# Performance work log

Hardware: AMD Instinct MI355X
Metric: run time of the kernel (lower is better)

The kernel has to match this reference:

```python
import jax, jax.numpy as jnp
import numpy as np

B, C, H, W, K = 4, 32, 192, 192, 3
BETA = 15.0   # soft-max temperature used by the repo's Morphology module
EPS = 1e-5    # BatchNorm eps
KK = K * K


def _window_taps(x, dil):
    """Zero-padded dilated KxK window taps, stacked on axis 0 -> (KK, B, C, H, W).
    Matches nn.Unfold(kernel_size=K, dilation=dil, padding=dil*(K//2))."""
    p = dil * (K // 2)
    xp = jnp.pad(x, ((0, 0), (0, 0), (p, p), (p, p)))
    return jnp.stack(
        [xp[:, :, i * dil:i * dil + H, j * dil:j * dil + W]
         for i in range(K) for j in range(K)], axis=0)


def _w_taps(w):
    # (C, K, K) -> (KK, 1, C, 1, 1) aligned with tap order i*K+j
    return w.reshape(C, KK).T[:, None, :, None, None]


def soft_dilate(x, w, dil):
    v = _window_taps(x, dil) + _w_taps(w)          # (KK,B,C,H,W)
    return jax.nn.logsumexp(BETA * v, axis=0) / BETA


def soft_erode(x, w, dil):
    v = _w_taps(w) - _window_taps(x, dil)
    return -(jax.nn.logsumexp(BETA * v, axis=0) / BETA)


def batchnorm(x, gamma, beta):
    mu = jnp.mean(x, axis=(0, 2, 3), keepdims=True)
    var = jnp.var(x, axis=(0, 2, 3), keepdims=True)
    xn = (x - mu) * jax.lax.rsqrt(var + EPS)
    return xn * gamma[None, :, None, None] + beta[None, :, None, None]


def setup_inputs() -> dict:
    key = jax.random.key(0)
    k1, k2, k3, k4 = jax.random.split(key, 4)
    return {
        "x": jax.random.normal(k1, (B, C, H, W), jnp.float32),
        "wd": jax.random.normal(k2, (4, C, K, K), jnp.float32) * 0.1,
        "we": jax.random.normal(k3, (4, C, K, K), jnp.float32) * 0.1,
        "gs": jnp.ones((4, C), jnp.float32),
        "bs": jnp.zeros((4, C), jnp.float32),
        "Wc": jax.random.normal(k4, (C, 4 * C), jnp.float32) * (1.0 / np.sqrt(4 * C)),
        "g": jnp.ones((C,), jnp.float32),
        "b": jnp.zeros((C,), jnp.float32),
    }


def reference(x, wd, we, gs, bs, Wc, g, b):
    branches = []
    for i in range(4):                      # fixed set of dilation factors 1..4
        d = i + 1
        y = soft_dilate(x, wd[i], d)        # soft morphological dilation
        y = soft_erode(y, we[i], d)         # then erosion => closing
        y = jax.nn.relu(batchnorm(y, gs[i], bs[i]))
        branches.append(y)
    xc = jnp.concatenate(branches, axis=1)  # (B, 4C, H, W)
    y = jnp.einsum('bihw,oi->bohw', xc, Wc) # 1x1 conv, no bias
    y = jax.nn.relu(batchnorm(y, g, b))
    return y                                 # Dropout2d is identity in eval
```

## Files before the change

kernel.cpp:

```cpp
#include <hip/hip_runtime.h>
#include <hip/hip_bf16.h>

#define B_   4
#define C_   32
#define H_   192
#define W_   192
#define HW_  (H_ * W_)
#define EPS_ 1e-5f

#define SCALE_IN  21.640425613334453f
#define SCALE_OUT 0.046209812037329687f

#define SPW 48
#define SQW 40

#define NP1 (128 * 576)
#define NP2 (32 * 288)

__device__ __forceinline__ float bf2f(unsigned short u) {
    return __uint_as_float((unsigned int)u << 16);
}
__device__ __forceinline__ unsigned short f2bf(float f) {
    const unsigned int u = __float_as_uint(f);
    return (unsigned short)((u + 0x7fffu + ((u >> 16) & 1u)) >> 16);
}

__device__ float          g_cw[2304];
__device__ float          g_Wt[4096];
__device__ float          g_stats[320];
__device__ float          g_p1[2 * NP1];
__device__ float          g_p2[2 * NP2];
__device__ __attribute__((aligned(16))) unsigned short g_E[(size_t)4 * B_ * C_ * HW_];
__device__ __attribute__((aligned(16))) unsigned short g_Yb[(size_t)B_ * C_ * HW_];

__global__ void prep_k(const float* __restrict__ wd, const float* __restrict__ we,
                       const float* __restrict__ Wc) {
    for (int i = threadIdx.x; i < 2304; i += 256) {
        const float v = (i < 1152) ? wd[i] : we[i - 1152];
        g_cw[i] = exp2f(SCALE_IN * v);
    }
    for (int i = threadIdx.x; i < 4096; i += 256) {
        const int ci = i >> 5;
        const int k  = i & 31;
        g_Wt[i] = Wc[(size_t)k * 128 + ci];
    }
}

template<int D>
__device__ __forceinline__ void morph_branch(int b, int c, int h0, int w0,
                                             int slotbase,
                                             const float* __restrict__ sP,
                                             float* __restrict__ sQ) {
    constexpr int QE   = 32 + 2 * D;
    constexpr int QEG  = (QE + 3) / 4;
    constexpr int UNITS = QE * QEG;
    constexpr int POFF = 8 - 2 * D;
    constexpr int AB   = POFF & ~3;
    constexpr int OFF  = POFF & 3;
    constexpr int NR   = (OFF + 2 * D + 4 + 3) / 4;
    constexpr int NR3  = (2 * D + 4 + 3) / 4;
    constexpr int br   = D - 1;

    const int tid = threadIdx.x;
    const int cb  = (br * C_ + c) * 9;

    {
        float cd[9];
#pragma unroll
        for (int k = 0; k < 9; k++) cd[k] = g_cw[cb + k];

#pragma unroll
        for (int it = 0; it < 2; ++it) {
            const int unit = tid + it * 256;
            if (unit < UNITS) {
                const int qi = unit / QEG;
                const int qj = (unit - qi * QEG) * 4;
                float a0 = 0.f, a1 = 0.f, a2 = 0.f, a3 = 0.f;
#pragma unroll
                for (int i = 0; i < 3; i++) {
                    const float* rp = &sP[(qi + 8 + (i - 2) * D) * SPW + qj + AB];
                    float buf[NR * 4];
#pragma unroll
                    for (int r = 0; r < NR; r++)
                        *(float4*)&buf[r * 4] = *(const float4*)&rp[r * 4];
#pragma unroll
                    for (int j = 0; j < 3; j++) {
                        const float wgt = cd[i * 3 + j];
                        a0 = fmaf(wgt, buf[OFF + j * D + 0], a0);
                        a1 = fmaf(wgt, buf[OFF + j * D + 1], a1);
                        a2 = fmaf(wgt, buf[OFF + j * D + 2], a2);
                        a3 = fmaf(wgt, buf[OFF + j * D + 3], a3);
                    }
                }
                float q0 = __builtin_amdgcn_rcpf(a0);
                float q1 = __builtin_amdgcn_rcpf(a1);
                float q2 = __builtin_amdgcn_rcpf(a2);
                float q3 = __builtin_amdgcn_rcpf(a3);
                const int hq = h0 - D + qi;
                const int wq = w0 - D + qj;
                const bool rowo = (hq < 0) || (hq >= H_);
                q0 = (rowo || (wq + 0 < 0) || (wq + 0 >= W_)) ? 1.0f : q0;
                q1 = (rowo || (wq + 1 < 0) || (wq + 1 >= W_)) ? 1.0f : q1;
                q2 = (rowo || (wq + 2 < 0) || (wq + 2 >= W_)) ? 1.0f : q2;
                q3 = (rowo || (wq + 3 < 0) || (wq + 3 >= W_)) ? 1.0f : q3;
                *(float4*)&sQ[qi * SQW + qj] = make_float4(q0, q1, q2, q3);
            }
        }
    }
    __syncthreads();

    {
        float ce[9];
#pragma unroll
        for (int k = 0; k < 9; k++) ce[k] = g_cw[1152 + cb + k];

        const int oi = tid >> 3;
        const int oj = (tid & 7) * 4;
        float t0 = 0.f, t1 = 0.f, t2 = 0.f, t3 = 0.f;
#pragma unroll
        for (int i = 0; i < 3; i++) {
            const float* rq = &sQ[(oi + i * D) * SQW + oj];
            float buf[NR3 * 4];
#pragma unroll
            for (int r = 0; r < NR3; r++)
                *(float4*)&buf[r * 4] = *(const float4*)&rq[r * 4];
#pragma unroll
            for (int j = 0; j < 3; j++) {
                const float wgt = ce[i * 3 + j];
                t0 = fmaf(wgt, buf[j * D + 0], t0);
                t1 = fmaf(wgt, buf[j * D + 1], t1);
                t2 = fmaf(wgt, buf[j * D + 2], t2);
                t3 = fmaf(wgt, buf[j * D + 3], t3);
            }
        }
        const float e0 = -SCALE_OUT * log2f(t0);
        const float e1 = -SCALE_OUT * log2f(t1);
        const float e2 = -SCALE_OUT * log2f(t2);
        const float e3 = -SCALE_OUT * log2f(t3);

        ushort4 r4;
        r4.x = f2bf(e0); r4.y = f2bf(e1); r4.z = f2bf(e2); r4.w = f2bf(e3);
        *(ushort4*)&g_E[(((size_t)br * B_ + b) * C_ + c) * HW_
                        + (size_t)(h0 + oi) * W_ + w0 + oj] = r4;

        float s1 = e0 + e1 + e2 + e3;
        float s2 = e0 * e0 + e1 * e1 + e2 * e2 + e3 * e3;
#pragma unroll
        for (int off = 32; off >= 1; off >>= 1) {
            s1 += __shfl_down(s1, off, 64);
            s2 += __shfl_down(s2, off, 64);
        }
        if ((tid & 63) == 0) {
            const int slot = (br * C_ + c) * 576 + slotbase + (tid >> 6);
            g_p1[slot]       = s1;
            g_p1[NP1 + slot] = s2;
        }
    }
    __syncthreads();
}

__global__ __launch_bounds__(256) void morph_k(const float* __restrict__ x) {
    __shared__ float sP[48 * SPW];
    __shared__ float sQ[40 * SQW];
    const int tile = blockIdx.x;
    const int c    = blockIdx.y;
    const int b    = blockIdx.z;
    const int th   = tile / 6;
    const int tw   = tile - th * 6;
    const int h0   = th * 32, w0 = tw * 32;

    const float* xm = x + (size_t)(b * C_ + c) * HW_;
    for (int idx = threadIdx.x; idx < 48 * 48; idx += 256) {
        const int r  = idx / 48, q = idx - r * 48;
        const int ih = h0 - 8 + r, iw = w0 - 8 + q;
        const int ihc = min(max(ih, 0), H_ - 1);
        const int iwc = min(max(iw, 0), W_ - 1);
        const float xv = xm[ihc * W_ + iwc];
        const bool inb = (ih == ihc) && (iw == iwc);
        sP[r * SPW + q] = inb ? exp2f(SCALE_IN * xv) : 1.0f;
    }
    __syncthreads();

    const int slotbase = (b * 36 + tile) * 4;
    morph_branch<1>(b, c, h0, w0, slotbase, sP, sQ);
    morph_branch<2>(b, c, h0, w0, slotbase, sP, sQ);
    morph_branch<3>(b, c, h0, w0, slotbase, sP, sQ);
    morph_branch<4>(b, c, h0, w0, slotbase, sP, sQ);
}

__global__ __launch_bounds__(256) void fin1_k(const float* __restrict__ gs,
                                              const float* __restrict__ bs) {
    const int chan = blockIdx.x;
    const int base = chan * 576;
    float s1 = 0.0f, s2 = 0.0f;
    for (int i = threadIdx.x; i < 576; i += 256) {
        s1 += g_p1[base + i];
        s2 += g_p1[NP1 + base + i];
    }
#pragma unroll
    for (int off = 32; off >= 1; off >>= 1) {
        s1 += __shfl_down(s1, off, 64);
        s2 += __shfl_down(s2, off, 64);
    }
    __shared__ float l1[4], l2[4];
    const int lane = threadIdx.x & 63;
    const int wv   = threadIdx.x >> 6;
    if (lane == 0) { l1[wv] = s1; l2[wv] = s2; }
    __syncthreads();
    if (threadIdx.x == 0) {
        const float S1 = l1[0] + l1[1] + l1[2] + l1[3];
        const float S2 = l2[0] + l2[1] + l2[2] + l2[3];
        const float N  = (float)(B_ * HW_);
        const float mu = S1 / N;
        const float va = fmaxf(S2 / N - mu * mu, 0.0f);
        const float sc = gs[chan] * rsqrtf(va + EPS_);
        g_stats[chan]       = sc;
        g_stats[128 + chan] = bs[chan] - mu * sc;
    }
}

__global__ __launch_bounds__(256) void conv_k(void) {
    const int og = blockIdx.y;
    const int b  = blockIdx.z;
    const int p  = (blockIdx.x * 256 + threadIdx.x) * 2;

    float acc0[8], acc1[8];
#pragma unroll
    for (int k = 0; k < 8; k++) { acc0[k] = 0.0f; acc1[k] = 0.0f; }

#pragma unroll 8
    for (int ci = 0; ci < 128; ci++) {
        const int br = ci >> 5;
        const int c  = ci & 31;
        const unsigned int eu =
            *(const unsigned int*)&g_E[(((size_t)br * B_ + b) * C_ + c) * HW_ + p];
        float v0 = __uint_as_float(eu << 16);
        float v1 = __uint_as_float(eu & 0xffff0000u);
        const float sc = g_stats[ci], sh = g_stats[128 + ci];
        v0 = fmaxf(fmaf(v0, sc, sh), 0.0f);
        v1 = fmaxf(fmaf(v1, sc, sh), 0.0f);
        const float* wr = &g_Wt[ci * 32 + og * 8];
#pragma unroll
        for (int k = 0; k < 8; k++) {
            acc0[k] = fmaf(v0, wr[k], acc0[k]);
            acc1[k] = fmaf(v1, wr[k], acc1[k]);
        }
    }

    unsigned short* Yp = g_Yb + ((size_t)b * C_ + og * 8) * HW_ + p;
#pragma unroll
    for (int k = 0; k < 8; k++) {
        const unsigned int pack =
            (unsigned int)f2bf(acc0[k]) | ((unsigned int)f2bf(acc1[k]) << 16);
        *(unsigned int*)&Yp[(size_t)k * HW_] = pack;
    }

    __shared__ float l1[8][4], l2[8][4];
    const int lane = threadIdx.x & 63;
    const int wv   = threadIdx.x >> 6;
#pragma unroll
    for (int k = 0; k < 8; k++) {
        float s1 = acc0[k] + acc1[k];
        float s2 = acc0[k] * acc0[k] + acc1[k] * acc1[k];
#pragma unroll
        for (int off = 32; off >= 1; off >>= 1) {
            s1 += __shfl_down(s1, off, 64);
            s2 += __shfl_down(s2, off, 64);
        }
        if (lane == 0) { l1[k][wv] = s1; l2[k][wv] = s2; }
    }
    __syncthreads();
    if (threadIdx.x < 8) {
        const int k = threadIdx.x;
        const int chan = og * 8 + k;
        const int slot = chan * 288 + b * 72 + blockIdx.x;
        g_p2[slot]       = l1[k][0] + l1[k][1] + l1[k][2] + l1[k][3];
        g_p2[NP2 + slot] = l2[k][0] + l2[k][1] + l2[k][2] + l2[k][3];
    }
}

__global__ __launch_bounds__(256) void fin2_k(const float* __restrict__ g,
                                              const float* __restrict__ bb) {
    const int chan = blockIdx.x;
    const int base = chan * 288;
    float s1 = 0.0f, s2 = 0.0f;
    for (int i = threadIdx.x; i < 288; i += 256) {
        s1 += g_p2[base + i];
        s2 += g_p2[NP2 + base + i];
    }
#pragma unroll
    for (int off = 32; off >= 1; off >>= 1) {
        s1 += __shfl_down(s1, off, 64);
        s2 += __shfl_down(s2, off, 64);
    }
    __shared__ float l1[4], l2[4];
    const int lane = threadIdx.x & 63;
    const int wv   = threadIdx.x >> 6;
    if (lane == 0) { l1[wv] = s1; l2[wv] = s2; }
    __syncthreads();
    if (threadIdx.x == 0) {
        const float S1 = l1[0] + l1[1] + l1[2] + l1[3];
        const float S2 = l2[0] + l2[1] + l2[2] + l2[3];
        const float N  = (float)(B_ * HW_);
        const float mu = S1 / N;
        const float va = fmaxf(S2 / N - mu * mu, 0.0f);
        const float sc = g[chan] * rsqrtf(va + EPS_);
        g_stats[256 + chan] = sc;
        g_stats[288 + chan] = bb[chan] - mu * sc;
    }
}

__global__ __launch_bounds__(256) void final_k(float* __restrict__ out) {
    const int c = blockIdx.y;
    const int b = blockIdx.z;
    const size_t base = (size_t)(b * C_ + c) * HW_ + (blockIdx.x * 256 + threadIdx.x) * 8;
    const float sc = g_stats[256 + c];
    const float sh = g_stats[288 + c];
    const uint4 u = *(const uint4*)&g_Yb[base];

    float4 r0, r1;
    r0.x = fmaxf(fmaf(__uint_as_float(u.x << 16),        sc, sh), 0.0f);
    r0.y = fmaxf(fmaf(__uint_as_float(u.x & 0xffff0000u), sc, sh), 0.0f);
    r0.z = fmaxf(fmaf(__uint_as_float(u.y << 16),        sc, sh), 0.0f);
    r0.w = fmaxf(fmaf(__uint_as_float(u.y & 0xffff0000u), sc, sh), 0.0f);
    r1.x = fmaxf(fmaf(__uint_as_float(u.z << 16),        sc, sh), 0.0f);
    r1.y = fmaxf(fmaf(__uint_as_float(u.z & 0xffff0000u), sc, sh), 0.0f);
    r1.z = fmaxf(fmaf(__uint_as_float(u.w << 16),        sc, sh), 0.0f);
    r1.w = fmaxf(fmaf(__uint_as_float(u.w & 0xffff0000u), sc, sh), 0.0f);

    *(float4*)&out[base]     = r0;
    *(float4*)&out[base + 4] = r1;
}

extern "C" void kernel_launch(void* const* d_in, const int* in_sizes, int n_in,
                              void* d_out, int out_size, void* d_ws, size_t ws_size,
                              hipStream_t stream) {
    const float* x  = (const float*)d_in[0];
    const float* wd = (const float*)d_in[1];
    const float* we = (const float*)d_in[2];
    const float* gs = (const float*)d_in[3];
    const float* bs = (const float*)d_in[4];
    const float* Wc = (const float*)d_in[5];
    const float* g  = (const float*)d_in[6];
    const float* bb = (const float*)d_in[7];

    prep_k<<<1, 256, 0, stream>>>(wd, we, Wc);
    morph_k<<<dim3(36, C_, B_), 256, 0, stream>>>(x);
    fin1_k<<<128, 256, 0, stream>>>(gs, bs);
    conv_k<<<dim3(HW_ / 512, 4, B_), 256, 0, stream>>>();
    fin2_k<<<32, 256, 0, stream>>>(g, bb);
    final_k<<<dim3(HW_ / 2048, C_, B_), 256, 0, stream>>>((float*)d_out);
}
```

Before: 101.2 us.

## Fold prep and fin2 kernels into neighbors and vectorize interior tile loads

Removes the single-block prep kernel by computing exp2 of the morphology weights inline in morph_k and building the transposed conv weight inside fin1_k. Folds the fin2 statistics reduction into final_k, where each block redundantly reduces its channel's partial sums. Adds a float4 halo-load path for interior column tiles. The aim is to cut two kernel launches and their serialization gaps, at the cost of redundant per-block reductions and exp2 work.

After: 99.91 us. Within noise of the previous version (-1.3%).

```diff
diff --git a/kernel.cpp b/kernel.cpp
--- a/kernel.cpp
+++ b/kernel.cpp
@@ -25,41 +25,29 @@
     return (unsigned short)((u + 0x7fffu + ((u >> 16) & 1u)) >> 16);
 }
 
-__device__ float          g_cw[2304];
 __device__ float          g_Wt[4096];
-__device__ float          g_stats[320];
+__device__ float          g_stats[256];
 __device__ float          g_p1[2 * NP1];
 __device__ float          g_p2[2 * NP2];
 __device__ __attribute__((aligned(16))) unsigned short g_E[(size_t)4 * B_ * C_ * HW_];
 __device__ __attribute__((aligned(16))) unsigned short g_Yb[(size_t)B_ * C_ * HW_];
 
-__global__ void prep_k(const float* __restrict__ wd, const float* __restrict__ we,
-                       const float* __restrict__ Wc) {
-    for (int i = threadIdx.x; i < 2304; i += 256) {
-        const float v = (i < 1152) ? wd[i] : we[i - 1152];
-        g_cw[i] = exp2f(SCALE_IN * v);
-    }
-    for (int i = threadIdx.x; i < 4096; i += 256) {
-        const int ci = i >> 5;
-        const int k  = i & 31;
-        g_Wt[i] = Wc[(size_t)k * 128 + ci];
-    }
-}
-
 template<int D>
-__device__ __forceinline__ void morph_branch(int b, int c, int h0, int w0,
+__device__ __forceinline__ void morph_branch(const float* __restrict__ wd,
+                                             const float* __restrict__ we,
+                                             int b, int c, int h0, int w0,
                                              int slotbase,
                                              const float* __restrict__ sP,
                                              float* __restrict__ sQ) {
-    constexpr int QE   = 32 + 2 * D;
-    constexpr int QEG  = (QE + 3) / 4;
+    constexpr int QE    = 32 + 2 * D;
+    constexpr int QEG   = (QE + 3) / 4;
     constexpr int UNITS = QE * QEG;
-    constexpr int POFF = 8 - 2 * D;
-    constexpr int AB   = POFF & ~3;
-    constexpr int OFF  = POFF & 3;
-    constexpr int NR   = (OFF + 2 * D + 4 + 3) / 4;
-    constexpr int NR3  = (2 * D + 4 + 3) / 4;
-    constexpr int br   = D - 1;
+    constexpr int POFF  = 8 - 2 * D;
+    constexpr int AB    = POFF & ~3;
+    constexpr int OFF   = POFF & 3;
+    constexpr int NR    = (OFF + 2 * D + 4 + 3) / 4;
+    constexpr int NR3   = (2 * D + 4 + 3) / 4;
+    constexpr int br    = D - 1;
 
     const int tid = threadIdx.x;
     const int cb  = (br * C_ + c) * 9;
@@ -67,7 +55,7 @@
     {
         float cd[9];
 #pragma unroll
-        for (int k = 0; k < 9; k++) cd[k] = g_cw[cb + k];
+        for (int k = 0; k < 9; k++) cd[k] = exp2f(SCALE_IN * wd[cb + k]);
 
 #pragma unroll
         for (int it = 0; it < 2; ++it) {
@@ -112,7 +100,7 @@
     {
         float ce[9];
 #pragma unroll
-        for (int k = 0; k < 9; k++) ce[k] = g_cw[1152 + cb + k];
+        for (int k = 0; k < 9; k++) ce[k] = exp2f(SCALE_IN * we[cb + k]);
 
         const int oi = tid >> 3;
         const int oj = (tid & 7) * 4;
@@ -159,7 +147,9 @@
     __syncthreads();
 }
 
-__global__ __launch_bounds__(256) void morph_k(const float* __restrict__ x) {
+__global__ __launch_bounds__(256) void morph_k(const float* __restrict__ x,
+                                               const float* __restrict__ wd,
+                                               const float* __restrict__ we) {
     __shared__ float sP[48 * SPW];
     __shared__ float sQ[40 * SQW];
     const int tile = blockIdx.x;
@@ -170,27 +160,54 @@
     const int h0   = th * 32, w0 = tw * 32;
 
     const float* xm = x + (size_t)(b * C_ + c) * HW_;
-    for (int idx = threadIdx.x; idx < 48 * 48; idx += 256) {
-        const int r  = idx / 48, q = idx - r * 48;
-        const int ih = h0 - 8 + r, iw = w0 - 8 + q;
-        const int ihc = min(max(ih, 0), H_ - 1);
-        const int iwc = min(max(iw, 0), W_ - 1);
-        const float xv = xm[ihc * W_ + iwc];
-        const bool inb = (ih == ihc) && (iw == iwc);
-        sP[r * SPW + q] = inb ? exp2f(SCALE_IN * xv) : 1.0f;
+    if (tw >= 1 && tw <= 4) {
+#pragma unroll
+        for (int pass = 0; pass < 3; ++pass) {
+            const int u = threadIdx.x + pass * 256;
+            if (u < 576) {
+                const int r  = u / 12;
+                const int q4 = (u - r * 12) * 4;
+                const int ih = h0 - 8 + r;
+                float4 v;
+                if (ih >= 0 && ih < H_) {
+                    const float4 xv = *(const float4*)&xm[ih * W_ + (w0 - 8 + q4)];
+                    v.x = exp2f(SCALE_IN * xv.x);
+                    v.y = exp2f(SCALE_IN * xv.y);
+                    v.z = exp2f(SCALE_IN * xv.z);
+                    v.w = exp2f(SCALE_IN * xv.w);
+                } else {
+                    v = make_float4(1.f, 1.f, 1.f, 1.f);
+                }
+                *(float4*)&sP[r * SPW + q4] = v;
+            }
+        }
+    } else {
+        for (int idx = threadIdx.x; idx < 48 * 48; idx += 256) {
+            const int r  = idx / 48, q = idx - r * 48;
+            const int ih = h0 - 8 + r, iw = w0 - 8 + q;
+            const int ihc = min(max(ih, 0), H_ - 1);
+            const int iwc = min(max(iw, 0), W_ - 1);
+            const float xv = xm[ihc * W_ + iwc];
+            const bool inb = (ih == ihc) && (iw == iwc);
+            sP[r * SPW + q] = inb ? exp2f(SCALE_IN * xv) : 1.0f;
+        }
     }
     __syncthreads();
 
     const int slotbase = (b * 36 + tile) * 4;
-    morph_branch<1>(b, c, h0, w0, slotbase, sP, sQ);
-    morph_branch<2>(b, c, h0, w0, slotbase, sP, sQ);
-    morph_branch<3>(b, c, h0, w0, slotbase, sP, sQ);
-    morph_branch<4>(b, c, h0, w0, slotbase, sP, sQ);
+    morph_branch<1>(wd, we, b, c, h0, w0, slotbase, sP, sQ);
+    morph_branch<2>(wd, we, b, c, h0, w0, slotbase, sP, sQ);
+    morph_branch<3>(wd, we, b, c, h0, w0, slotbase, sP, sQ);
+    morph_branch<4>(wd, we, b, c, h0, w0, slotbase, sP, sQ);
 }
 
 __global__ __launch_bounds__(256) void fin1_k(const float* __restrict__ gs,
-                                              const float* __restrict__ bs) {
+                                              const float* __restrict__ bs,
+                                              const float* __restrict__ Wc) {
     const int chan = blockIdx.x;
+    if (threadIdx.x < 32)
+        g_Wt[chan * 32 + threadIdx.x] = Wc[(size_t)threadIdx.x * 128 + chan];
+
     const int base = chan * 576;
     float s1 = 0.0f, s2 = 0.0f;
     for (int i = threadIdx.x; i < 576; i += 256) {
@@ -279,53 +296,56 @@
     }
 }
 
-__global__ __launch_bounds__(256) void fin2_k(const float* __restrict__ g,
-                                              const float* __restrict__ bb) {
-    const int chan = blockIdx.x;
-    const int base = chan * 288;
-    float s1 = 0.0f, s2 = 0.0f;
-    for (int i = threadIdx.x; i < 288; i += 256) {
-        s1 += g_p2[base + i];
-        s2 += g_p2[NP2 + base + i];
-    }
-#pragma unroll
-    for (int off = 32; off >= 1; off >>= 1) {
-        s1 += __shfl_down(s1, off, 64);
-        s2 += __shfl_down(s2, off, 64);
-    }
-    __shared__ float l1[4], l2[4];
-    const int lane = threadIdx.x & 63;
-    const int wv   = threadIdx.x >> 6;
-    if (lane == 0) { l1[wv] = s1; l2[wv] = s2; }
-    __syncthreads();
-    if (threadIdx.x == 0) {
-        const float S1 = l1[0] + l1[1] + l1[2] + l1[3];
-        const float S2 = l2[0] + l2[1] + l2[2] + l2[3];
-        const float N  = (float)(B_ * HW_);
-        const float mu = S1 / N;
-        const float va = fmaxf(S2 / N - mu * mu, 0.0f);
-        const float sc = g[chan] * rsqrtf(va + EPS_);
-        g_stats[256 + chan] = sc;
-        g_stats[288 + chan] = bb[chan] - mu * sc;
-    }
-}
-
-__global__ __launch_bounds__(256) void final_k(float* __restrict__ out) {
+__global__ __launch_bounds__(256) void final_k(const float* __restrict__ g,
+                                               const float* __restrict__ bb,
+                                               float* __restrict__ out) {
     const int c = blockIdx.y;
     const int b = blockIdx.z;
+
+    __shared__ float l1[4], l2[4];
+    __shared__ float sScSh[2];
+    {
+        const int base = c * 288;
+        float s1 = 0.0f, s2 = 0.0f;
+        for (int i = threadIdx.x; i < 288; i += 256) {
+            s1 += g_p2[base + i];
+            s2 += g_p2[NP2 + base + i];
+        }
+#pragma unroll
+        for (int off = 32; off >= 1; off >>= 1) {
+            s1 += __shfl_down(s1, off, 64);
+            s2 += __shfl_down(s2, off, 64);
+        }
+        const int lane = threadIdx.x & 63;
+        const int wv   = threadIdx.x >> 6;
+        if (lane == 0) { l1[wv] = s1; l2[wv] = s2; }
+        __syncthreads();
+        if (threadIdx.x == 0) {
+            const float S1 = l1[0] + l1[1] + l1[2] + l1[3];
+            const float S2 = l2[0] + l2[1] + l2[2] + l2[3];
+            const float N  = (float)(B_ * HW_);
+            const float mu = S1 / N;
+            const float va = fmaxf(S2 / N - mu * mu, 0.0f);
+            const float sc = g[c] * rsqrtf(va + EPS_);
+            sScSh[0] = sc;
+            sScSh[1] = bb[c] - mu * sc;
+        }
+        __syncthreads();
+    }
+    const float sc = sScSh[0];
+    const float sh = sScSh[1];
+
     const size_t base = (size_t)(b * C_ + c) * HW_ + (blockIdx.x * 256 + threadIdx.x) * 8;
-    const float sc = g_stats[256 + c];
-    const float sh = g_stats[288 + c];
     const uint4 u = *(const uint4*)&g_Yb[base];
 
     float4 r0, r1;
-    r0.x = fmaxf(fmaf(__uint_as_float(u.x << 16),        sc, sh), 0.0f);
+    r0.x = fmaxf(fmaf(__uint_as_float(u.x << 16),         sc, sh), 0.0f);
     r0.y = fmaxf(fmaf(__uint_as_float(u.x & 0xffff0000u), sc, sh), 0.0f);
-    r0.z = fmaxf(fmaf(__uint_as_float(u.y << 16),        sc, sh), 0.0f);
+    r0.z = fmaxf(fmaf(__uint_as_float(u.y << 16),         sc, sh), 0.0f);
     r0.w = fmaxf(fmaf(__uint_as_float(u.y & 0xffff0000u), sc, sh), 0.0f);
-    r1.x = fmaxf(fmaf(__uint_as_float(u.z << 16),        sc, sh), 0.0f);
+    r1.x = fmaxf(fmaf(__uint_as_float(u.z << 16),         sc, sh), 0.0f);
     r1.y = fmaxf(fmaf(__uint_as_float(u.z & 0xffff0000u), sc, sh), 0.0f);
-    r1.z = fmaxf(fmaf(__uint_as_float(u.w << 16),        sc, sh), 0.0f);
+    r1.z = fmaxf(fmaf(__uint_as_float(u.w << 16),         sc, sh), 0.0f);
     r1.w = fmaxf(fmaf(__uint_as_float(u.w & 0xffff0000u), sc, sh), 0.0f);
 
     *(float4*)&out[base]     = r0;
@@ -344,10 +364,8 @@
     const float* g  = (const float*)d_in[6];
     const float* bb = (const float*)d_in[7];
 
-    prep_k<<<1, 256, 0, stream>>>(wd, we, Wc);
-    morph_k<<<dim3(36, C_, B_), 256, 0, stream>>>(x);
-    fin1_k<<<128, 256, 0, stream>>>(gs, bs);
+    morph_k<<<dim3(36, C_, B_), 256, 0, stream>>>(x, wd, we);
+    fin1_k<<<128, 256, 0, stream>>>(gs, bs, Wc);
     conv_k<<<dim3(HW_ / 512, 4, B_), 256, 0, stream>>>();
-    fin2_k<<<32, 256, 0, stream>>>(g, bb);
-    final_k<<<dim3(HW_ / 2048, C_, B_), 256, 0, stream>>>((float*)d_out);
-}
+    final_k<<<dim3(HW_ / 2048, C_, B_), 256, 0, stream>>>(g, bb, (float*)d_out);
+}
```
